# Optimization experiments

Measured on AMD Instinct MI355X. Metric: run time of the kernel, lower is better.

The kernel has to match this reference:

```python
import jax, jax.numpy as jnp
import numpy as np

GRID_SIZE = 5
SPLINE_ORDER = 3
NUM_BASIS = GRID_SIZE + SPLINE_ORDER  # 8


def make_grid():
    # knots: grid_size + 2*spline_order + 1 = 12 points over extended [-1,1]
    h = 2.0 / GRID_SIZE
    return (jnp.arange(-SPLINE_ORDER, GRID_SIZE + SPLINE_ORDER + 1, dtype=jnp.float32) * h - 1.0)[None, :]  # (1, 12)


def b_splines(x, grid):
    # x: (N, in) -> bases: (N, in, NUM_BASIS) via Cox-de Boor recursion
    x = x[..., None]  # (N, in, 1)
    bases = ((x >= grid[:, :-1]) & (x < grid[:, 1:])).astype(x.dtype)
    for p in range(1, SPLINE_ORDER + 1):
        left = (x - grid[:, : -(p + 1)]) / (grid[:, p:-1] - grid[:, : -(p + 1)])
        right = (grid[:, p + 1:] - x) / (grid[:, p + 1:] - grid[:, 1:-p])
        bases = left * bases[..., :-1] + right * bases[..., 1:]
    return bases


def kan_linear(x, base_w, spline_w, scaler, grid):
    # x: (N, in); base_w: (out, in); spline_w: (out, in, G); scaler: (out, in)
    base = jnp.einsum('ni,oi->no', jax.nn.silu(x), base_w)
    bases = b_splines(x, grid)  # (N, in, G)
    spline = jnp.einsum('nig,oig->no', bases, spline_w * scaler[..., None])
    return base + spline


def setup_inputs() -> dict:
    key = jax.random.key(0)
    ks = jax.random.split(key, 7)
    H, L = 768, 2
    hidden = jax.random.normal(ks[0], (32, 512, H), dtype=jnp.float32)
    s = 0.1
    return {
        'hidden': hidden,
        'base_w1': jax.random.normal(ks[1], (H, H), jnp.float32) * s,
        'spline_w1': jax.random.normal(ks[2], (H, H, NUM_BASIS), jnp.float32) * s,
        'scaler1': jax.random.normal(ks[3], (H, H), jnp.float32) * s + 1.0,
        'base_w2': jax.random.normal(ks[4], (L, H), jnp.float32) * s,
        'spline_w2': jax.random.normal(ks[5], (L, H, NUM_BASIS), jnp.float32) * s,
        'scaler2': jax.random.normal(ks[6], (L, H), jnp.float32) * s + 1.0,
    }


def reference(hidden, base_w1, spline_w1, scaler1, base_w2, spline_w2, scaler2):
    grid = make_grid()
    B, S, H = hidden.shape
    x = hidden.reshape(-1, H)  # (N, H)
    x = kan_linear(x, base_w1, spline_w1, scaler1, grid)
    x = jax.nn.gelu(x, approximate=False)  # torch F.gelu default = erf
    out = kan_linear(x, base_w2, spline_w2, scaler2, grid)  # (N, L)
    return out.reshape(B, S, -1).squeeze(-1) if out.shape[-1] == 1 else out.reshape(B, S, -1)
```

## Files before the change

### kernel.cpp

```cpp
#include <hip/hip_runtime.h>
#include <math.h>

#define NROWS 16384
#define H     768
#define KEXP  6912
#define NCHUNK 108
#define NITER 54

typedef __attribute__((ext_vector_type(8))) short  bhalf8;
typedef __attribute__((ext_vector_type(4))) float  floatx4;

__device__ __forceinline__ unsigned short f2bf(float f) {
    unsigned int u = __float_as_uint(f);
    u = (u + 0x7FFFu + ((u >> 16) & 1u)) >> 16;
    return (unsigned short)u;
}
__device__ __forceinline__ float bf2f(unsigned short h) {
    return __uint_as_float(((unsigned int)h) << 16);
}
__device__ __forceinline__ unsigned int pack2(unsigned short a, unsigned short b) {
    return (unsigned int)a | ((unsigned int)b << 16);
}
__device__ __forceinline__ float silu_f(float x) { return x / (1.0f + __expf(-x)); }

__device__ __forceinline__ float gelu_fast(float x) {
    float x3 = x * x * x;
    float y = fmaf(x3, 0.0356774081f, x * 0.7978845608f);
    float e = __expf(2.0f * y);
    float th = 1.0f - 2.0f / (e + 1.0f);
    return 0.5f * x * (1.0f + th);
}

__device__ __forceinline__ void kan_bases(float x, float* __restrict__ b) {
    const float c6 = 0.166666666667f;
    float u  = fmaf(x, 2.5f, 5.5f);
    float fj = floorf(u);
    float t  = u - fj;
    int  j0  = (int)fj;
    float t2 = t * t, t3 = t2 * t;
    float n0 = t3 * c6;
    float n1 = fmaf(t3, -0.5f, fmaf(t2, 0.5f, fmaf(t, 0.5f, c6)));
    float n2 = fmaf(t3, 0.5f, fmaf(t2, -1.0f, 0.666666666667f));
    float omt = 1.0f - t;
    float n3 = omt * omt * omt * c6;
#pragma unroll
    for (int c = 0; c < 8; ++c) {
        int d = j0 - c;
        float v = (d == 0) ? n0 : 0.0f;
        v = (d == 1) ? n1 : v;
        v = (d == 2) ? n2 : v;
        v = (d == 3) ? n3 : v;
        b[c] = v;
    }
}

__global__ __launch_bounds__(256) void prep_expand(
    const float* __restrict__ x, const float* __restrict__ bw,
    const float* __restrict__ sw, const float* __restrict__ sc,
    unsigned short* __restrict__ wp, unsigned short* __restrict__ F)
{
    const int b = blockIdx.x, t = threadIdx.x;
    if (b < H) {
        const int n = b;
        const float* bwr = bw + (size_t)n * H;
        unsigned short* out = wp + (size_t)n * KEXP;
        if (t < 96) {
            const float4* xp = (const float4*)(bwr + t * 8);
            float4 v0 = xp[0], v1 = xp[1];
            uint4 pk;
            pk.x = pack2(f2bf(v0.x), f2bf(v0.y));
            pk.y = pack2(f2bf(v0.z), f2bf(v0.w));
            pk.z = pack2(f2bf(v1.x), f2bf(v1.y));
            pk.w = pack2(f2bf(v1.z), f2bf(v1.w));
            *(uint4*)(out + t * 8) = pk;
        }
#pragma unroll
        for (int p = 0; p < 3; ++p) {
            int i = t + p * 256;
            float s = sc[(size_t)n * H + i];
            const float4* swp = (const float4*)(sw + ((size_t)n * H + i) * 8);
            float4 w0 = swp[0], w1 = swp[1];
            uint4 pk;
            pk.x = pack2(f2bf(w0.x * s), f2bf(w0.y * s));
            pk.y = pack2(f2bf(w0.z * s), f2bf(w0.w * s));
            pk.z = pack2(f2bf(w1.x * s), f2bf(w1.y * s));
            pk.w = pack2(f2bf(w1.z * s), f2bf(w1.w * s));
            *(uint4*)(out + H + (size_t)i * 8) = pk;
        }
    } else {
        const int n = b - H;
        __shared__ float sX[H];
        const float* xr = x + (size_t)n * H;
        if (t < 192) ((float4*)sX)[t] = ((const float4*)xr)[t];
        __syncthreads();
        unsigned short* out = F + (size_t)n * KEXP;
        if (t < 96) {
            const float4* xp = (const float4*)(sX + t * 8);
            float4 v0 = xp[0], v1 = xp[1];
            uint4 pk;
            pk.x = pack2(f2bf(silu_f(v0.x)), f2bf(silu_f(v0.y)));
            pk.y = pack2(f2bf(silu_f(v0.z)), f2bf(silu_f(v0.w)));
            pk.z = pack2(f2bf(silu_f(v1.x)), f2bf(silu_f(v1.y)));
            pk.w = pack2(f2bf(silu_f(v1.z)), f2bf(silu_f(v1.w)));
            *(uint4*)(out + t * 8) = pk;
        }
#pragma unroll
        for (int p = 0; p < 3; ++p) {
            int i = t + p * 256;
            float xv = sX[i];
            float bb[8];
            kan_bases(xv, bb);
            uint4 pk;
            pk.x = pack2(f2bf(bb[0]), f2bf(bb[1]));
            pk.y = pack2(f2bf(bb[2]), f2bf(bb[3]));
            pk.z = pack2(f2bf(bb[4]), f2bf(bb[5]));
            pk.w = pack2(f2bf(bb[6]), f2bf(bb[7]));
            *(uint4*)(out + H + (size_t)i * 8) = pk;
        }
    }
}


#define AS1 __attribute__((address_space(1)))
#define AS3 __attribute__((address_space(3)))

#define DSR(D, A, O) asm volatile("ds_read_b128 %0, %1 offset:" #O : "=v"(D) : "v"(A) : "memory")
#define LDA0(O) do{ DSR(fA0[0],avA[0],O); DSR(fA0[1],avA[1],O); DSR(fA0[2],avA[2],O); DSR(fA0[3],avA[3],O); \
                    DSR(fA0[4],avA[4],O); DSR(fA0[5],avA[5],O); DSR(fA0[6],avA[6],O); DSR(fA0[7],avA[7],O); }while(0)
#define LDA1(O) do{ DSR(fA1[0],avA[0],O); DSR(fA1[1],avA[1],O); DSR(fA1[2],avA[2],O); DSR(fA1[3],avA[3],O); \
                    DSR(fA1[4],avA[4],O); DSR(fA1[5],avA[5],O); DSR(fA1[6],avA[6],O); DSR(fA1[7],avA[7],O); }while(0)
#define LDB(O)  do{ DSR(fB[0],avB[0],O); DSR(fB[1],avB[1],O); }while(0)

#define MM0(QN) do{ \
    _Pragma("unroll") \
    for (int kk = 0; kk < 2; ++kk) \
        _Pragma("unroll") \
        for (int im = 0; im < 4; ++im) \
            acc0[QN][im] = __builtin_amdgcn_mfma_f32_16x16x32_bf16( \
                fA0[im*2+kk], fB[kk], acc0[QN][im], 0, 0, 0); \
}while(0)
#define MM1(QN) do{ \
    _Pragma("unroll") \
    for (int kk = 0; kk < 2; ++kk) \
        _Pragma("unroll") \
        for (int im = 0; im < 4; ++im) \
            acc1[QN][im] = __builtin_amdgcn_mfma_f32_16x16x32_bf16( \
                fA1[im*2+kk], fB[kk], acc1[QN][im], 0, 0, 0); \
}while(0)

#define STG_A(BF,HH,KS) do{ \
    __builtin_amdgcn_global_load_lds((const AS1 void*)(pA##HH[0] + (size_t)(KS)*64), \
        (AS3 void*)&sA[BF][HH][wb8], 16, 0, 0); \
    __builtin_amdgcn_global_load_lds((const AS1 void*)(pA##HH[1] + (size_t)(KS)*64), \
        (AS3 void*)&sA[BF][HH][4096 + wb8], 16, 0, 0); \
}while(0)
#define STG_B(BF,QN,KS) \
    __builtin_amdgcn_global_load_lds((const AS1 void*)(pB[QN] + (size_t)(KS)*64), \
        (AS3 void*)&sB[BF][QN][wb8], 16, 0, 0)

#define PH_MID do{ __builtin_amdgcn_s_barrier(); \
    asm volatile("s_waitcnt lgkmcnt(0)" ::: "memory"); \
    __builtin_amdgcn_sched_barrier(0); \
    __builtin_amdgcn_s_setprio(1); }while(0)
#define PH_END do{ __builtin_amdgcn_s_setprio(0); \
    __builtin_amdgcn_sched_barrier(0); \
    __builtin_amdgcn_s_barrier(); }while(0)
#define PH_END_VMN(N) do{ __builtin_amdgcn_s_setprio(0); \
    __builtin_amdgcn_sched_barrier(0); \
    asm volatile("s_waitcnt vmcnt(" #N ")" ::: "memory"); \
    __builtin_amdgcn_s_barrier(); }while(0)

__global__ __launch_bounds__(512, 2) void kan1_gemm(
    const unsigned short* __restrict__ F, const unsigned short* __restrict__ wp,
    unsigned short* __restrict__ l1)
{
    __shared__ __align__(16) unsigned short sA[2][2][8192];
    __shared__ __align__(16) unsigned short sB[2][3][4096];

    const int b = blockIdx.x;
    const int s = b >> 3;
    const int rowT = (b & 7) * 8 + (s >> 2);
    const int colT = s & 3;
    const int rowBase = rowT * 256, colBase = colT * 192;

    const int t = threadIdx.x;
    const int lane = t & 63;
    const int quad = lane >> 4, lm = lane & 15, p7 = lane & 7;
    const int wv = t >> 6, wr = wv & 1, wc = wv >> 1;

    const int rr = t >> 3;
    const int slotx = (t & 7) ^ (rr & 7);
    const int wb8 = (t & 448) * 8;

    const unsigned short* pA0[2]; const unsigned short* pA1[2];
    const unsigned short* pB[3];
#pragma unroll
    for (int p = 0; p < 2; ++p) {
        pA0[p] = F + (size_t)(rowBase +       p*64 + rr) * KEXP + slotx*8;
        pA1[p] = F + (size_t)(rowBase + 128 + p*64 + rr) * KEXP + slotx*8;
    }
#pragma unroll
    for (int q = 0; q < 3; ++q)
        pB[q] = wp + (size_t)(colBase + q*64 + rr) * KEXP + slotx*8;

    unsigned int avA[8], avB[2];
    {
        unsigned int aB = (unsigned int)(size_t)(AS3 unsigned short*)&sA[0][0][0];
        unsigned int bB = (unsigned int)(size_t)(AS3 unsigned short*)&sB[0][0][0];
#pragma unroll
        for (int im = 0; im < 4; ++im)
#pragma unroll
            for (int kk = 0; kk < 2; ++kk)
                avA[im*2+kk] = aB + (unsigned)(((wr*64 + im*16 + lm)*64 + (((kk*4+quad)^p7)*8)) * 2);
#pragma unroll
        for (int kk = 0; kk < 2; ++kk)
            avB[kk] = bB + (unsigned)(((wc*16 + lm)*64 + (((kk*4+quad)^p7)*8)) * 2);
    }

    floatx4 acc0[3][4] = {};
    floatx4 acc1[3][4] = {};
    bhalf8 fA0[8], fA1[8], fB[2];

    STG_A(0,0,0); STG_A(0,1,0); STG_B(0,0,0); STG_B(0,1,0); STG_B(0,2,0);
    STG_A(1,0,1); STG_A(1,1,1); STG_B(1,0,1); STG_B(1,1,1);
    asm volatile("s_waitcnt vmcnt(8)" ::: "memory");
    __builtin_amdgcn_s_barrier();

#pragma unroll 1
    for (int i = 0; i < NITER; ++i) {
        const int k1 = 2*i + 1;
        const int k2 = (2*i + 2 > 107) ? 107 : 2*i + 2;
        const int k3 = (2*i + 3 > 107) ? 107 : 2*i + 3;
        LDA0(0);     LDB(0);     STG_B(1,2,k1);               PH_MID; MM0(0);         PH_END_VMN(10);
        LDA1(16384);             STG_A(0,0,k2);               PH_MID; MM1(0);         PH_END_VMN(10);
        LDB(8192);               STG_A(0,1,k2);               PH_MID; MM1(1); MM0(1); PH_END_VMN(11);
        LDB(16384);              STG_B(0,0,k2); STG_B(0,1,k2);PH_MID; MM0(2); MM1(2); PH_END_VMN(8);
        LDA0(32768); LDB(24576); STG_B(0,2,k2);               PH_MID; MM0(0);         PH_END;
        LDA1(49152);             STG_A(1,0,k3);               PH_MID; MM1(0);         PH_END_VMN(10);
        LDB(32768);              STG_A(1,1,k3);               PH_MID; MM1(1); MM0(1); PH_END_VMN(11);
        LDB(40960);              STG_B(1,0,k3); STG_B(1,1,k3);PH_MID; MM0(2); MM1(2); PH_END_VMN(8);
    }

#pragma unroll
    for (int qn = 0; qn < 3; ++qn)
#pragma unroll
    for (int im = 0; im < 4; ++im) {
        const int col = colBase + qn*64 + wc*16 + lm;
        {
            const int row0 = rowBase + wr*64 + im*16 + quad*4;
#pragma unroll
            for (int rg = 0; rg < 4; ++rg)
                l1[(size_t)(row0 + rg) * H + col] = f2bf(acc0[qn][im][rg]);
        }
        {
            const int row0 = rowBase + 128 + wr*64 + im*16 + quad*4;
#pragma unroll
            for (int rg = 0; rg < 4; ++rg)
                l1[(size_t)(row0 + rg) * H + col] = f2bf(acc1[qn][im][rg]);
        }
    }
}

__global__ __launch_bounds__(256) void kan2_kernel(
    const unsigned short* __restrict__ l1, const float* __restrict__ bw,
    const float* __restrict__ sw, const float* __restrict__ sc,
    float* __restrict__ out)
{
    const int lane = threadIdx.x & 63;
    const int wv = threadIdx.x >> 6;
    const int n = blockIdx.x * 4 + wv;
    float a0 = 0.f, a1 = 0.f;
#pragma unroll
    for (int ii = 0; ii < H / 64; ++ii) {
        int i = lane + ii * 64;
        float h = bf2f(l1[(size_t)n * H + i]);
        float u = gelu_fast(h);
        float f0 = silu_f(u);
        float bb[8];
        kan_bases(u, bb);
        float bw0 = bw[i], bw1 = bw[H + i];
        float s0 = sc[i], s1 = sc[H + i];
        const float4* q0 = (const float4*)(sw + (size_t)i * 8);
        const float4* q1 = (const float4*)(sw + (size_t)(H + i) * 8);
        float4 w00 = q0[0], w01 = q0[1];
        float4 w10 = q1[0], w11 = q1[1];
        float t0 = bb[0]*w00.x + bb[1]*w00.y + bb[2]*w00.z + bb[3]*w00.w
                 + bb[4]*w01.x + bb[5]*w01.y + bb[6]*w01.z + bb[7]*w01.w;
        float t1 = bb[0]*w10.x + bb[1]*w10.y + bb[2]*w10.z + bb[3]*w10.w
                 + bb[4]*w11.x + bb[5]*w11.y + bb[6]*w11.z + bb[7]*w11.w;
        a0 += f0 * bw0 + s0 * t0;
        a1 += f0 * bw1 + s1 * t1;
    }
#pragma unroll
    for (int off = 32; off > 0; off >>= 1) {
        a0 += __shfl_down(a0, off, 64);
        a1 += __shfl_down(a1, off, 64);
    }
    if (lane == 0) {
        out[(size_t)n * 2 + 0] = a0;
        out[(size_t)n * 2 + 1] = a1;
    }
}

extern "C" void kernel_launch(void* const* d_in, const int* in_sizes, int n_in,
                              void* d_out, int out_size, void* d_ws, size_t ws_size,
                              hipStream_t stream) {
    const float* hidden = (const float*)d_in[0];
    const float* bw1    = (const float*)d_in[1];
    const float* sw1    = (const float*)d_in[2];
    const float* sc1    = (const float*)d_in[3];
    const float* bw2    = (const float*)d_in[4];
    const float* sw2    = (const float*)d_in[5];
    const float* sc2    = (const float*)d_in[6];
    float* out = (float*)d_out;

    const size_t l1_elems = (size_t)NROWS * H;
    const size_t wp_elems = (size_t)H * KEXP;
    unsigned short* l1 = (unsigned short*)d_ws;
    unsigned short* wp = l1 + l1_elems;
    unsigned short* F  = wp + wp_elems;

    prep_expand<<<H + NROWS, 256, 0, stream>>>(hidden, bw1, sw1, sc1, wp, F);
    kan1_gemm<<<256, 512, 0, stream>>>(F, wp, l1);
    kan2_kernel<<<NROWS / 4, 256, 0, stream>>>(l1, bw2, sw2, sc2, out);
}
```

Measured before the change: 336.4 us.

## Flatten prep kernel grid and stage layer-2 weights in LDS as bf16

The input-expansion prep now uses three blocks per row, one element per thread, with no shared-memory staging or barrier, and the weight-packing blocks move to the end of the grid. The layer-2 kernel packs the scaled spline weights and base weights into LDS as bf16 once per block and processes 16 rows per block instead of 4, which removes repeated global/L2 fetches of fp32 weights. This trades extra LDS setup per block and bf16 rounding of the layer-2 weights for less global traffic. The per-thread silu store in prep becomes a scalar 2-byte write instead of a vectorised one.

Result: slower. 396.7 us (+17.9%).

```diff
diff --git a/kernel.cpp b/kernel.cpp
--- a/kernel.cpp
+++ b/kernel.cpp
@@ -54,14 +54,29 @@
     }
 }
 
-__global__ __launch_bounds__(256) void prep_expand(
+__global__ __launch_bounds__(256) void prep_flat(
     const float* __restrict__ x, const float* __restrict__ bw,
     const float* __restrict__ sw, const float* __restrict__ sc,
     unsigned short* __restrict__ wp, unsigned short* __restrict__ F)
 {
     const int b = blockIdx.x, t = threadIdx.x;
-    if (b < H) {
-        const int n = b;
+    if (b < 3 * NROWS) {
+        const int n = b / 3;
+        const int seg = b - n * 3;
+        const int i = seg * 256 + t;
+        float xv = x[(size_t)n * H + i];
+        unsigned short* out = F + (size_t)n * KEXP;
+        out[i] = f2bf(silu_f(xv));
+        float bb[8];
+        kan_bases(xv, bb);
+        uint4 pk;
+        pk.x = pack2(f2bf(bb[0]), f2bf(bb[1]));
+        pk.y = pack2(f2bf(bb[2]), f2bf(bb[3]));
+        pk.z = pack2(f2bf(bb[4]), f2bf(bb[5]));
+        pk.w = pack2(f2bf(bb[6]), f2bf(bb[7]));
+        *(uint4*)(out + H + (size_t)i * 8) = pk;
+    } else {
+        const int n = b - 3 * NROWS;
         const float* bwr = bw + (size_t)n * H;
         unsigned short* out = wp + (size_t)n * KEXP;
         if (t < 96) {
@@ -85,36 +100,6 @@
             pk.y = pack2(f2bf(w0.z * s), f2bf(w0.w * s));
             pk.z = pack2(f2bf(w1.x * s), f2bf(w1.y * s));
             pk.w = pack2(f2bf(w1.z * s), f2bf(w1.w * s));
-            *(uint4*)(out + H + (size_t)i * 8) = pk;
-        }
-    } else {
-        const int n = b - H;
-        __shared__ float sX[H];
-        const float* xr = x + (size_t)n * H;
-        if (t < 192) ((float4*)sX)[t] = ((const float4*)xr)[t];
-        __syncthreads();
-        unsigned short* out = F + (size_t)n * KEXP;
-        if (t < 96) {
-            const float4* xp = (const float4*)(sX + t * 8);
-            float4 v0 = xp[0], v1 = xp[1];
-            uint4 pk;
-            pk.x = pack2(f2bf(silu_f(v0.x)), f2bf(silu_f(v0.y)));
-            pk.y = pack2(f2bf(silu_f(v0.z)), f2bf(silu_f(v0.w)));
-            pk.z = pack2(f2bf(silu_f(v1.x)), f2bf(silu_f(v1.y)));
-            pk.w = pack2(f2bf(silu_f(v1.z)), f2bf(silu_f(v1.w)));
-            *(uint4*)(out + t * 8) = pk;
-        }
-#pragma unroll
-        for (int p = 0; p < 3; ++p) {
-            int i = t + p * 256;
-            float xv = sX[i];
-            float bb[8];
-            kan_bases(xv, bb);
-            uint4 pk;
-            pk.x = pack2(f2bf(bb[0]), f2bf(bb[1]));
-            pk.y = pack2(f2bf(bb[2]), f2bf(bb[3]));
-            pk.z = pack2(f2bf(bb[4]), f2bf(bb[5]));
-            pk.w = pack2(f2bf(bb[6]), f2bf(bb[7]));
             *(uint4*)(out + H + (size_t)i * 8) = pk;
         }
     }
@@ -261,44 +246,75 @@
     }
 }
 
+#define R2 16
 __global__ __launch_bounds__(256) void kan2_kernel(
     const unsigned short* __restrict__ l1, const float* __restrict__ bw,
     const float* __restrict__ sw, const float* __restrict__ sc,
     float* __restrict__ out)
 {
-    const int lane = threadIdx.x & 63;
-    const int wv = threadIdx.x >> 6;
-    const int n = blockIdx.x * 4 + wv;
-    float a0 = 0.f, a1 = 0.f;
-#pragma unroll
-    for (int ii = 0; ii < H / 64; ++ii) {
-        int i = lane + ii * 64;
-        float h = bf2f(l1[(size_t)n * H + i]);
-        float u = gelu_fast(h);
-        float f0 = silu_f(u);
-        float bb[8];
-        kan_bases(u, bb);
-        float bw0 = bw[i], bw1 = bw[H + i];
-        float s0 = sc[i], s1 = sc[H + i];
-        const float4* q0 = (const float4*)(sw + (size_t)i * 8);
-        const float4* q1 = (const float4*)(sw + (size_t)(H + i) * 8);
-        float4 w00 = q0[0], w01 = q0[1];
-        float4 w10 = q1[0], w11 = q1[1];
-        float t0 = bb[0]*w00.x + bb[1]*w00.y + bb[2]*w00.z + bb[3]*w00.w
-                 + bb[4]*w01.x + bb[5]*w01.y + bb[6]*w01.z + bb[7]*w01.w;
-        float t1 = bb[0]*w10.x + bb[1]*w10.y + bb[2]*w10.z + bb[3]*w10.w
-                 + bb[4]*w11.x + bb[5]*w11.y + bb[6]*w11.z + bb[7]*w11.w;
-        a0 += f0 * bw0 + s0 * t0;
-        a1 += f0 * bw1 + s1 * t1;
-    }
-#pragma unroll
-    for (int off = 32; off > 0; off >>= 1) {
-        a0 += __shfl_down(a0, off, 64);
-        a1 += __shfl_down(a1, off, 64);
-    }
-    if (lane == 0) {
-        out[(size_t)n * 2 + 0] = a0;
-        out[(size_t)n * 2 + 1] = a1;
+    __shared__ __align__(16) unsigned short sW[2 * H * 8];
+    __shared__ unsigned int sB2[H];
+
+    const int t = threadIdx.x;
+#pragma unroll
+    for (int c = 0; c < 6; ++c) {
+        int idx = t + c * 256;
+        int o = (idx >= H) ? 1 : 0;
+        int i = idx - o * H;
+        float s = sc[(size_t)o * H + i];
+        const float4* q = (const float4*)(sw + ((size_t)o * H + i) * 8);
+        float4 w0 = q[0], w1 = q[1];
+        uint4 pk;
+        pk.x = pack2(f2bf(w0.x * s), f2bf(w0.y * s));
+        pk.y = pack2(f2bf(w0.z * s), f2bf(w0.w * s));
+        pk.z = pack2(f2bf(w1.x * s), f2bf(w1.y * s));
+        pk.w = pack2(f2bf(w1.z * s), f2bf(w1.w * s));
+        *(uint4*)&sW[(size_t)idx * 8] = pk;
+    }
+#pragma unroll
+    for (int c = 0; c < 3; ++c) {
+        int i = t + c * 256;
+        sB2[i] = pack2(f2bf(bw[i]), f2bf(bw[H + i]));
+    }
+    __syncthreads();
+
+    const int lane = t & 63;
+    const int wv = t >> 6;
+#pragma unroll 1
+    for (int r = 0; r < 4; ++r) {
+        const int n = blockIdx.x * R2 + wv * 4 + r;
+        float a0 = 0.f, a1 = 0.f;
+#pragma unroll
+        for (int ii = 0; ii < H / 64; ++ii) {
+            int i = lane + ii * 64;
+            float h = bf2f(l1[(size_t)n * H + i]);
+            float u = gelu_fast(h);
+            float f0 = silu_f(u);
+            float bb[8];
+            kan_bases(u, bb);
+            unsigned int bp = sB2[i];
+            float bw0 = bf2f((unsigned short)(bp & 0xffffu));
+            float bw1 = bf2f((unsigned short)(bp >> 16));
+            bhalf8 w0 = *(const bhalf8*)&sW[(size_t)i * 8];
+            bhalf8 w1 = *(const bhalf8*)&sW[(size_t)(H + i) * 8];
+            float t0 = 0.f, t1 = 0.f;
+#pragma unroll
+            for (int c = 0; c < 8; ++c) {
+                t0 = fmaf(bb[c], bf2f((unsigned short)w0[c]), t0);
+                t1 = fmaf(bb[c], bf2f((unsigned short)w1[c]), t1);
+            }
+            a0 += fmaf(f0, bw0, t0);
+            a1 += fmaf(f0, bw1, t1);
+        }
+#pragma unroll
+        for (int off = 32; off > 0; off >>= 1) {
+            a0 += __shfl_down(a0, off, 64);
+            a1 += __shfl_down(a1, off, 64);
+        }
+        if (lane == 0) {
+            out[(size_t)n * 2 + 0] = a0;
+            out[(size_t)n * 2 + 1] = a1;
+        }
     }
 }
 
@@ -320,7 +336,7 @@
     unsigned short* wp = l1 + l1_elems;
     unsigned short* F  = wp + wp_elems;
 
-    prep_expand<<<H + NROWS, 256, 0, stream>>>(hidden, bw1, sw1, sc1, wp, F);
+    prep_flat<<<3 * NROWS + H, 256, 0, stream>>>(hidden, bw1, sw1, sc1, wp, F);
     kan1_gemm<<<256, 512, 0, stream>>>(F, wp, l1);
-    kan2_kernel<<<NROWS / 4, 256, 0, stream>>>(l1, bw2, sw2, sc2, out);
-}
+    kan2_kernel<<<NROWS / R2, 256, 0, stream>>>(l1, bw2, sw2, sc2, out);
+}
```

## Fuse B-spline basis expansion into GEMM A-tile staging via LDS writes

Applied to the files above, without the earlier changes.

Previously the full expanded feature matrix F (16384 x 6912 bf16) was written to global memory and streamed back by the GEMM. Now only the SiLU part is precomputed. The spline bases are computed inside the GEMM from raw fp32 inputs, using a shift-based granule packer, and written straight into LDS. This cuts a large global write and read, at the cost of extra ALU work and a restructured two-phase pipeline. Launch bounds drop to 1 block per CU in min-blocks terms.

Result: slower. 386.2 us (+14.8%).

```diff
diff --git a/kernel.cpp b/kernel.cpp
--- a/kernel.cpp
+++ b/kernel.cpp
@@ -5,10 +5,10 @@
 #define H     768
 #define KEXP  6912
 #define NCHUNK 108
-#define NITER 54
 
 typedef __attribute__((ext_vector_type(8))) short  bhalf8;
 typedef __attribute__((ext_vector_type(4))) float  floatx4;
+typedef __attribute__((ext_vector_type(4))) unsigned int uintx4;
 
 __device__ __forceinline__ unsigned short f2bf(float f) {
     unsigned int u = __float_as_uint(f);
@@ -54,14 +54,55 @@
     }
 }
 
-__global__ __launch_bounds__(256) void prep_expand(
+__device__ __forceinline__ uintx4 expand_granule(float xv) {
+    const float c6 = 0.166666666667f;
+    float u  = fmaf(xv, 2.5f, 5.5f);
+    float fj = floorf(u);
+    float t  = u - fj;
+    int  j0  = (int)fj;
+    float t2 = t * t, t3 = t2 * t;
+    float n0 = t3 * c6;
+    float n1 = fmaf(t3, -0.5f, fmaf(t2, 0.5f, fmaf(t, 0.5f, c6)));
+    float n2 = fmaf(t3, 0.5f, fmaf(t2, -1.0f, 0.666666666667f));
+    float omt = 1.0f - t;
+    float n3 = omt * omt * omt * c6;
+    unsigned long long P = (unsigned long long)pack2(f2bf(n3), f2bf(n2))
+                         | ((unsigned long long)pack2(f2bf(n1), f2bf(n0)) << 32);
+    int sh = 16 * (j0 - 3);
+    bool a0 = (sh >= 0) & (sh < 64);
+    bool a1 = (sh >= 64) & (sh < 128);
+    bool a2 = (sh > -64) & (sh < 0);
+    int shl = sh & 63;
+    unsigned long long t0  = P << shl;
+    unsigned long long t0h = shl ? (P >> (64 - shl)) : 0ull;
+    unsigned long long t1  = P << ((sh - 64) & 63);
+    unsigned long long t2l = P >> ((-sh) & 63);
+    unsigned long long lo = a0 ? t0  : (a2 ? t2l : 0ull);
+    unsigned long long hi = a0 ? t0h : (a1 ? t1  : 0ull);
+    uintx4 o;
+    o.x = (unsigned int)lo; o.y = (unsigned int)(lo >> 32);
+    o.z = (unsigned int)hi; o.w = (unsigned int)(hi >> 32);
+    return o;
+}
+
+__global__ __launch_bounds__(256) void prep_sw(
     const float* __restrict__ x, const float* __restrict__ bw,
     const float* __restrict__ sw, const float* __restrict__ sc,
-    unsigned short* __restrict__ wp, unsigned short* __restrict__ F)
+    unsigned short* __restrict__ wp, unsigned short* __restrict__ S)
 {
     const int b = blockIdx.x, t = threadIdx.x;
-    if (b < H) {
-        const int n = b;
+    if (b < 6144) {
+        const size_t i = ((size_t)b * 256 + t) * 8;
+        const float4* xp = (const float4*)(x + i);
+        float4 v0 = xp[0], v1 = xp[1];
+        uint4 pk;
+        pk.x = pack2(f2bf(silu_f(v0.x)), f2bf(silu_f(v0.y)));
+        pk.y = pack2(f2bf(silu_f(v0.z)), f2bf(silu_f(v0.w)));
+        pk.z = pack2(f2bf(silu_f(v1.x)), f2bf(silu_f(v1.y)));
+        pk.w = pack2(f2bf(silu_f(v1.z)), f2bf(silu_f(v1.w)));
+        *(uint4*)(S + i) = pk;
+    } else {
+        const int n = b - 6144;
         const float* bwr = bw + (size_t)n * H;
         unsigned short* out = wp + (size_t)n * KEXP;
         if (t < 96) {
@@ -87,36 +128,6 @@
             pk.w = pack2(f2bf(w1.z * s), f2bf(w1.w * s));
             *(uint4*)(out + H + (size_t)i * 8) = pk;
         }
-    } else {
-        const int n = b - H;
-        __shared__ float sX[H];
-        const float* xr = x + (size_t)n * H;
-        if (t < 192) ((float4*)sX)[t] = ((const float4*)xr)[t];
-        __syncthreads();
-        unsigned short* out = F + (size_t)n * KEXP;
-        if (t < 96) {
-            const float4* xp = (const float4*)(sX + t * 8);
-            float4 v0 = xp[0], v1 = xp[1];
-            uint4 pk;
-            pk.x = pack2(f2bf(silu_f(v0.x)), f2bf(silu_f(v0.y)));
-            pk.y = pack2(f2bf(silu_f(v0.z)), f2bf(silu_f(v0.w)));
-            pk.z = pack2(f2bf(silu_f(v1.x)), f2bf(silu_f(v1.y)));
-            pk.w = pack2(f2bf(silu_f(v1.z)), f2bf(silu_f(v1.w)));
-            *(uint4*)(out + t * 8) = pk;
-        }
-#pragma unroll
-        for (int p = 0; p < 3; ++p) {
-            int i = t + p * 256;
-            float xv = sX[i];
-            float bb[8];
-            kan_bases(xv, bb);
-            uint4 pk;
-            pk.x = pack2(f2bf(bb[0]), f2bf(bb[1]));
-            pk.y = pack2(f2bf(bb[2]), f2bf(bb[3]));
-            pk.z = pack2(f2bf(bb[4]), f2bf(bb[5]));
-            pk.w = pack2(f2bf(bb[6]), f2bf(bb[7]));
-            *(uint4*)(out + H + (size_t)i * 8) = pk;
-        }
     }
 }
 
@@ -125,6 +136,7 @@
 #define AS3 __attribute__((address_space(3)))
 
 #define DSR(D, A, O) asm volatile("ds_read_b128 %0, %1 offset:" #O : "=v"(D) : "v"(A) : "memory")
+#define DSW(A, D, O) asm volatile("ds_write_b128 %0, %1 offset:" #O :: "v"(A), "v"(D) : "memory")
 #define LDA0(O) do{ DSR(fA0[0],avA[0],O); DSR(fA0[1],avA[1],O); DSR(fA0[2],avA[2],O); DSR(fA0[3],avA[3],O); \
                     DSR(fA0[4],avA[4],O); DSR(fA0[5],avA[5],O); DSR(fA0[6],avA[6],O); DSR(fA0[7],avA[7],O); }while(0)
 #define LDA1(O) do{ DSR(fA1[0],avA[0],O); DSR(fA1[1],avA[1],O); DSR(fA1[2],avA[2],O); DSR(fA1[3],avA[3],O); \
@@ -148,15 +160,23 @@
                 fA1[im*2+kk], fB[kk], acc1[QN][im], 0, 0, 0); \
 }while(0)
 
-#define STG_A(BF,HH,KS) do{ \
-    __builtin_amdgcn_global_load_lds((const AS1 void*)(pA##HH[0] + (size_t)(KS)*64), \
+#define STG_SA(BF,HH,KS) do{ \
+    __builtin_amdgcn_global_load_lds((const AS1 void*)(pS##HH[0] + (size_t)(KS)*64), \
         (AS3 void*)&sA[BF][HH][wb8], 16, 0, 0); \
-    __builtin_amdgcn_global_load_lds((const AS1 void*)(pA##HH[1] + (size_t)(KS)*64), \
+    __builtin_amdgcn_global_load_lds((const AS1 void*)(pS##HH[1] + (size_t)(KS)*64), \
         (AS3 void*)&sA[BF][HH][4096 + wb8], 16, 0, 0); \
 }while(0)
 #define STG_B(BF,QN,KS) \
     __builtin_amdgcn_global_load_lds((const AS1 void*)(pB[QN] + (size_t)(KS)*64), \
         (AS3 void*)&sB[BF][QN][wb8], 16, 0, 0)
+
+#define EXPAND(XV, O) do{ \
+    uintx4 g0 = expand_granule(XV.x); \
+    uintx4 g1 = expand_granule(XV.y); \
+    uintx4 g2 = expand_granule(XV.z); \
+    uintx4 g3 = expand_granule(XV.w); \
+    DSW(aw0, g0, O); DSW(aw1, g1, O); DSW(aw2, g2, O); DSW(aw3, g3, O); \
+}while(0)
 
 #define PH_MID do{ __builtin_amdgcn_s_barrier(); \
     asm volatile("s_waitcnt lgkmcnt(0)" ::: "memory"); \
@@ -170,9 +190,9 @@
     asm volatile("s_waitcnt vmcnt(" #N ")" ::: "memory"); \
     __builtin_amdgcn_s_barrier(); }while(0)
 
-__global__ __launch_bounds__(512, 2) void kan1_gemm(
-    const unsigned short* __restrict__ F, const unsigned short* __restrict__ wp,
-    unsigned short* __restrict__ l1)
+__global__ __launch_bounds__(512, 1) void kan1_fused(
+    const unsigned short* __restrict__ S, const float* __restrict__ x,
+    const unsigned short* __restrict__ wp, unsigned short* __restrict__ l1)
 {
     __shared__ __align__(16) unsigned short sA[2][2][8192];
     __shared__ __align__(16) unsigned short sB[2][3][4096];
@@ -192,18 +212,23 @@
     const int slotx = (t & 7) ^ (rr & 7);
     const int wb8 = (t & 448) * 8;
 
-    const unsigned short* pA0[2]; const unsigned short* pA1[2];
+    const unsigned short* pS0[2]; const unsigned short* pS1[2];
     const unsigned short* pB[3];
 #pragma unroll
     for (int p = 0; p < 2; ++p) {
-        pA0[p] = F + (size_t)(rowBase +       p*64 + rr) * KEXP + slotx*8;
-        pA1[p] = F + (size_t)(rowBase + 128 + p*64 + rr) * KEXP + slotx*8;
+        pS0[p] = S + (size_t)(rowBase +       p*64 + rr) * H + slotx*8;
+        pS1[p] = S + (size_t)(rowBase + 128 + p*64 + rr) * H + slotx*8;
     }
 #pragma unroll
     for (int q = 0; q < 3; ++q)
         pB[q] = wp + (size_t)(colBase + q*64 + rr) * KEXP + slotx*8;
 
+    const int er  = t >> 1;
+    const int esb = (t & 1) * 4;
+    const float* pX = x + (size_t)(rowBase + er) * H + esb;
+
     unsigned int avA[8], avB[2];
+    unsigned int aw0, aw1, aw2, aw3;
     {
         unsigned int aB = (unsigned int)(size_t)(AS3 unsigned short*)&sA[0][0][0];
         unsigned int bB = (unsigned int)(size_t)(AS3 unsigned short*)&sB[0][0][0];
@@ -215,30 +240,70 @@
 #pragma unroll
         for (int kk = 0; kk < 2; ++kk)
             avB[kk] = bB + (unsigned)(((wc*16 + lm)*64 + (((kk*4+quad)^p7)*8)) * 2);
+        const int hh = er >> 7, rl = er & 127;
+        aw0 = aB + (unsigned)(hh*16384 + rl*128 + (((esb+0)^(er&7))*16));
+        aw1 = aB + (unsigned)(hh*16384 + rl*128 + (((esb+1)^(er&7))*16));
+        aw2 = aB + (unsigned)(hh*16384 + rl*128 + (((esb+2)^(er&7))*16));
+        aw3 = aB + (unsigned)(hh*16384 + rl*128 + (((esb+3)^(er&7))*16));
     }
 
     floatx4 acc0[3][4] = {};
     floatx4 acc1[3][4] = {};
     bhalf8 fA0[8], fA1[8], fB[2];
 
-    STG_A(0,0,0); STG_A(0,1,0); STG_B(0,0,0); STG_B(0,1,0); STG_B(0,2,0);
-    STG_A(1,0,1); STG_A(1,1,1); STG_B(1,0,1); STG_B(1,1,1);
-    asm volatile("s_waitcnt vmcnt(8)" ::: "memory");
+    STG_SA(0,0,0); STG_SA(0,1,0); STG_B(0,0,0); STG_B(0,1,0); STG_B(0,2,0);
+    asm volatile("s_waitcnt vmcnt(0)" ::: "memory");
     __builtin_amdgcn_s_barrier();
-
 #pragma unroll 1
-    for (int i = 0; i < NITER; ++i) {
-        const int k1 = 2*i + 1;
-        const int k2 = (2*i + 2 > 107) ? 107 : 2*i + 2;
-        const int k3 = (2*i + 3 > 107) ? 107 : 2*i + 3;
-        LDA0(0);     LDB(0);     STG_B(1,2,k1);               PH_MID; MM0(0);         PH_END_VMN(10);
-        LDA1(16384);             STG_A(0,0,k2);               PH_MID; MM1(0);         PH_END_VMN(10);
-        LDB(8192);               STG_A(0,1,k2);               PH_MID; MM1(1); MM0(1); PH_END_VMN(11);
-        LDB(16384);              STG_B(0,0,k2); STG_B(0,1,k2);PH_MID; MM0(2); MM1(2); PH_END_VMN(8);
-        LDA0(32768); LDB(24576); STG_B(0,2,k2);               PH_MID; MM0(0);         PH_END;
-        LDA1(49152);             STG_A(1,0,k3);               PH_MID; MM1(0);         PH_END_VMN(10);
-        LDB(32768);              STG_A(1,1,k3);               PH_MID; MM1(1); MM0(1); PH_END_VMN(11);
-        LDB(40960);              STG_B(1,0,k3); STG_B(1,1,k3);PH_MID; MM0(2); MM1(2); PH_END_VMN(8);
+    for (int ii = 0; ii < 6; ++ii) {
+        const int ko = 2*ii + 1, kn = 2*ii + 2;
+        STG_SA(1,0,ko); STG_SA(1,1,ko); STG_B(1,0,ko); STG_B(1,1,ko); STG_B(1,2,ko);
+        LDA0(0); LDB(0);      PH_MID; MM0(0);         PH_END;
+        LDA1(16384);          PH_MID; MM1(0);         PH_END;
+        LDB(8192);            PH_MID; MM1(1); MM0(1); PH_END;
+        LDB(16384);           PH_MID; MM0(2); MM1(2); PH_END_VMN(0);
+        if (ii < 5) { STG_SA(0,0,kn); STG_SA(0,1,kn); STG_B(0,0,kn); STG_B(0,1,kn); STG_B(0,2,kn); }
+        LDA0(32768); LDB(24576); PH_MID; MM0(0);         PH_END;
+        LDA1(49152);             PH_MID; MM1(0);         PH_END;
+        LDB(32768);              PH_MID; MM1(1); MM0(1); PH_END;
+        LDB(40960);              PH_MID; MM0(2); MM1(2); PH_END_VMN(0);
+    }
+
+    float4 xva = *(const float4*)(pX + 12*8 - 96);
+    float4 xvb = *(const float4*)(pX + 13*8 - 96);
+    STG_B(0,0,12); STG_B(0,1,12); STG_B(0,2,12);
+    STG_B(1,0,13); STG_B(1,1,13); STG_B(1,2,13);
+    EXPAND(xva, 0);
+    EXPAND(xvb, 32768);
+    asm volatile("s_waitcnt vmcnt(0) lgkmcnt(0)" ::: "memory");
+    __builtin_amdgcn_s_barrier();
+
+#pragma unroll 1
+    for (int i = 0; i < 48; ++i) {
+        const int ke = 12 + 2*i, ko = ke + 1;
+        const int k2e = ke + 2, k2o = ko + 2;
+        const bool pe = (k2e <= 107), po = (k2o <= 107);
+        LDA0(0); LDB(0);
+        if (pe) xva = *(const float4*)(pX + (size_t)k2e*8 - 96);
+                               PH_MID; MM0(0);         PH_END;
+        LDA1(16384);
+        if (pe) STG_B(0,0,k2e); PH_MID; MM1(0);        PH_END_VMN(5);
+        LDB(8192);
+        if (pe) STG_B(0,1,k2e);
+        EXPAND(xvb, 32768);     PH_MID; MM1(1); MM0(1); PH_END;
+        LDB(16384);
+        if (pe) STG_B(0,2,k2e); PH_MID; MM0(2); MM1(2); PH_END_VMN(6);
+        LDA0(32768); LDB(24576);
+        if (po) xvb = *(const float4*)(pX + (size_t)k2o*8 - 96);
+                               PH_MID; MM0(0);         PH_END;
+        LDA1(49152);
+        if (po) STG_B(1,0,k2o); PH_MID; MM1(0);        PH_END_VMN(5);
+        LDB(32768);
+        if (po) STG_B(1,1,k2o);
+        if (pe) { EXPAND(xva, 0); }
+                               PH_MID; MM1(1); MM0(1); PH_END;
+        LDB(40960);
+        if (po) STG_B(1,2,k2o); PH_MID; MM0(2); MM1(2); PH_END_VMN(6);
     }
 
 #pragma unroll
@@ -318,9 +383,9 @@
     const size_t wp_elems = (size_t)H * KEXP;
     unsigned short* l1 = (unsigned short*)d_ws;
     unsigned short* wp = l1 + l1_elems;
-    unsigned short* F  = wp + wp_elems;
-
-    prep_expand<<<H + NROWS, 256, 0, stream>>>(hidden, bw1, sw1, sc1, wp, F);
-    kan1_gemm<<<256, 512, 0, stream>>>(F, wp, l1);
+    unsigned short* S  = wp + wp_elems;
+
+    prep_sw<<<6144 + H, 256, 0, stream>>>(hidden, bw1, sw1, sc1, wp, S);
+    kan1_fused<<<256, 512, 0, stream>>>(S, hidden, wp, l1);
     kan2_kernel<<<NROWS / 4, 256, 0, stream>>>(l1, bw2, sw2, sc2, out);
 }
```

## Flatten feature expansion grid and merge GEMM phases into six fused MFMA steps

Applied to the files above, without the earlier changes.

The prep kernel now handles feature expansion with 6144 blocks that each process 2048 flat elements directly from global memory, with no shared-memory staging or per-row blocks. The weight-packing blocks move to the tail of the grid. In the GEMM main loop, eight barrier phases per iteration become six: both A fragment halves are read together and MM0/MM1 run in the same phase, with the vmcnt waits adjusted to match. This cuts barriers and launch blocks, but the per-element silu writes are now 2-byte scattered stores, and it raises register pressure from holding fA0 and fA1 at the same time.

After: 330.5 us. No clear change (-1.7%).

```diff
diff --git a/kernel.cpp b/kernel.cpp
--- a/kernel.cpp
+++ b/kernel.cpp
@@ -60,8 +60,27 @@
     unsigned short* __restrict__ wp, unsigned short* __restrict__ F)
 {
     const int b = blockIdx.x, t = threadIdx.x;
-    if (b < H) {
-        const int n = b;
+    if (b < 6144) {
+        const int e0 = b * 2048 + t;
+#pragma unroll
+        for (int j = 0; j < 8; ++j) {
+            int e = e0 + j * 256;
+            int n = e / 768;
+            int i = e - n * 768;
+            float xv = x[e];
+            unsigned short* out = F + (size_t)n * KEXP;
+            out[i] = f2bf(silu_f(xv));
+            float bb[8];
+            kan_bases(xv, bb);
+            uint4 pk;
+            pk.x = pack2(f2bf(bb[0]), f2bf(bb[1]));
+            pk.y = pack2(f2bf(bb[2]), f2bf(bb[3]));
+            pk.z = pack2(f2bf(bb[4]), f2bf(bb[5]));
+            pk.w = pack2(f2bf(bb[6]), f2bf(bb[7]));
+            *(uint4*)(out + H + (size_t)i * 8) = pk;
+        }
+    } else {
+        const int n = b - 6144;
         const float* bwr = bw + (size_t)n * H;
         unsigned short* out = wp + (size_t)n * KEXP;
         if (t < 96) {
@@ -85,36 +104,6 @@
             pk.y = pack2(f2bf(w0.z * s), f2bf(w0.w * s));
             pk.z = pack2(f2bf(w1.x * s), f2bf(w1.y * s));
             pk.w = pack2(f2bf(w1.z * s), f2bf(w1.w * s));
-            *(uint4*)(out + H + (size_t)i * 8) = pk;
-        }
-    } else {
-        const int n = b - H;
-        __shared__ float sX[H];
-        const float* xr = x + (size_t)n * H;
-        if (t < 192) ((float4*)sX)[t] = ((const float4*)xr)[t];
-        __syncthreads();
-        unsigned short* out = F + (size_t)n * KEXP;
-        if (t < 96) {
-            const float4* xp = (const float4*)(sX + t * 8);
-            float4 v0 = xp[0], v1 = xp[1];
-            uint4 pk;
-            pk.x = pack2(f2bf(silu_f(v0.x)), f2bf(silu_f(v0.y)));
-            pk.y = pack2(f2bf(silu_f(v0.z)), f2bf(silu_f(v0.w)));
-            pk.z = pack2(f2bf(silu_f(v1.x)), f2bf(silu_f(v1.y)));
-            pk.w = pack2(f2bf(silu_f(v1.z)), f2bf(silu_f(v1.w)));
-            *(uint4*)(out + t * 8) = pk;
-        }
-#pragma unroll
-        for (int p = 0; p < 3; ++p) {
-            int i = t + p * 256;
-            float xv = sX[i];
-            float bb[8];
-            kan_bases(xv, bb);
-            uint4 pk;
-            pk.x = pack2(f2bf(bb[0]), f2bf(bb[1]));
-            pk.y = pack2(f2bf(bb[2]), f2bf(bb[3]));
-            pk.z = pack2(f2bf(bb[4]), f2bf(bb[5]));
-            pk.w = pack2(f2bf(bb[6]), f2bf(bb[7]));
             *(uint4*)(out + H + (size_t)i * 8) = pk;
         }
     }
@@ -162,9 +151,6 @@
     asm volatile("s_waitcnt lgkmcnt(0)" ::: "memory"); \
     __builtin_amdgcn_sched_barrier(0); \
     __builtin_amdgcn_s_setprio(1); }while(0)
-#define PH_END do{ __builtin_amdgcn_s_setprio(0); \
-    __builtin_amdgcn_sched_barrier(0); \
-    __builtin_amdgcn_s_barrier(); }while(0)
 #define PH_END_VMN(N) do{ __builtin_amdgcn_s_setprio(0); \
     __builtin_amdgcn_sched_barrier(0); \
     asm volatile("s_waitcnt vmcnt(" #N ")" ::: "memory"); \
@@ -231,14 +217,18 @@
         const int k1 = 2*i + 1;
         const int k2 = (2*i + 2 > 107) ? 107 : 2*i + 2;
         const int k3 = (2*i + 3 > 107) ? 107 : 2*i + 3;
-        LDA0(0);     LDB(0);     STG_B(1,2,k1);               PH_MID; MM0(0);         PH_END_VMN(10);
-        LDA1(16384);             STG_A(0,0,k2);               PH_MID; MM1(0);         PH_END_VMN(10);
-        LDB(8192);               STG_A(0,1,k2);               PH_MID; MM1(1); MM0(1); PH_END_VMN(11);
-        LDB(16384);              STG_B(0,0,k2); STG_B(0,1,k2);PH_MID; MM0(2); MM1(2); PH_END_VMN(8);
-        LDA0(32768); LDB(24576); STG_B(0,2,k2);               PH_MID; MM0(0);         PH_END;
-        LDA1(49152);             STG_A(1,0,k3);               PH_MID; MM1(0);         PH_END_VMN(10);
-        LDB(32768);              STG_A(1,1,k3);               PH_MID; MM1(1); MM0(1); PH_END_VMN(11);
-        LDB(40960);              STG_B(1,0,k3); STG_B(1,1,k3);PH_MID; MM0(2); MM1(2); PH_END_VMN(8);
+        LDA0(0); LDA1(16384); LDB(0);
+        STG_B(1,2,k1);                 PH_MID; MM0(0); MM1(0); PH_END_VMN(8);
+        LDB(8192);
+        STG_A(0,0,k2); STG_A(0,1,k2);  PH_MID; MM0(1); MM1(1); PH_END_VMN(11);
+        LDB(16384);
+        STG_B(0,0,k2); STG_B(0,1,k2);  PH_MID; MM0(2); MM1(2); PH_END_VMN(8);
+        LDA0(32768); LDA1(49152); LDB(24576);
+        STG_B(0,2,k2);                 PH_MID; MM0(0); MM1(0); PH_END_VMN(8);
+        LDB(32768);
+        STG_A(1,0,k3); STG_A(1,1,k3);  PH_MID; MM0(1); MM1(1); PH_END_VMN(11);
+        LDB(40960);
+        STG_B(1,0,k3); STG_B(1,1,k3);  PH_MID; MM0(2); MM1(2); PH_END_VMN(8);
     }
 
 #pragma unroll
@@ -320,7 +310,7 @@
     unsigned short* wp = l1 + l1_elems;
     unsigned short* F  = wp + wp_elems;
 
-    prep_expand<<<H + NROWS, 256, 0, stream>>>(hidden, bw1, sw1, sc1, wp, F);
+    prep_expand<<<6144 + H, 256, 0, stream>>>(hidden, bw1, sw1, sc1, wp, F);
     kan1_gemm<<<256, 512, 0, stream>>>(F, wp, l1);
     kan2_kernel<<<NROWS / 4, 256, 0, stream>>>(l1, bw2, sw2, sc2, out);
 }
```
